# Optimization experiments

Measured on AMD Instinct MI355X. Metric: run time of the kernel, lower is better.

Reference implementation:

```python
import jax, jax.numpy as jnp
import numpy as np

D_MODEL = 1024
N_HEADS = 16
D_K = D_MODEL // N_HEADS
B, S = 2, 2048
NEG = -1.0e9


def setup_inputs() -> dict:
    key = jax.random.key(0)
    ks = jax.random.split(key, 12)
    sc = 1.0 / np.sqrt(D_MODEL)
    inp = {
        'query': jax.random.normal(ks[0], (B, S, D_MODEL), jnp.float32),
        'key': jax.random.normal(ks[1], (B, S, D_MODEL), jnp.float32),
        'value': jax.random.normal(ks[2], (B, S, D_MODEL), jnp.float32),
        # causal mask, broadcast over batch: 1 = attend, 0 = masked
        'mask': jnp.broadcast_to(jnp.tril(jnp.ones((S, S), jnp.int32)), (B, S, S)),
        'wq': jax.random.normal(ks[3], (D_MODEL, D_MODEL), jnp.float32) * sc,
        'bq': jnp.zeros((D_MODEL,), jnp.float32),
        'wk': jax.random.normal(ks[4], (D_MODEL, D_MODEL), jnp.float32) * sc,
        'bk': jnp.zeros((D_MODEL,), jnp.float32),
        'wv': jax.random.normal(ks[5], (D_MODEL, D_MODEL), jnp.float32) * sc,
        'bv': jnp.zeros((D_MODEL,), jnp.float32),
        'wo': jax.random.normal(ks[6], (D_MODEL, D_MODEL), jnp.float32) * sc,
        'bo': jnp.zeros((D_MODEL,), jnp.float32),
    }
    return inp


def reference(query, key, value, mask, wq, bq, wk, bk, wv, bv, wo, bo):
    b, sq, _ = query.shape
    sk = key.shape[1]
    # linear projections, split into heads: [B, H, S, d_k]
    def proj(x, w, bias, s):
        return (x @ w + bias).reshape(b, s, N_HEADS, D_K).transpose(0, 2, 1, 3)
    Q = proj(query, wq, bq, sq)
    K = proj(key, wk, bk, sk)
    V = proj(value, wv, bv, sk)
    # scaled dot-product attention with full score matrix [B, H, Sq, Sk]
    scores = jnp.einsum('bhqd,bhkd->bhqk', Q, K) / np.sqrt(D_K)
    scores = jnp.where(mask[:, None, :, :] == 0, NEG, scores)
    attn = jax.nn.softmax(scores, axis=-1)
    ctx = jnp.einsum('bhqk,bhkd->bhqd', attn, V)
    ctx = ctx.transpose(0, 2, 1, 3).reshape(b, sq, D_MODEL)
    return ctx @ wo + bo
```

## Files before the change

kernel.cpp:

```cpp
#include <hip/hip_runtime.h>
#include <stdint.h>

#define AS1 __attribute__((address_space(1)))
#define AS3 __attribute__((address_space(3)))

typedef __attribute__((ext_vector_type(8))) __bf16 bf16x8;
typedef __attribute__((ext_vector_type(4))) float f32x4;
typedef __attribute__((ext_vector_type(4))) unsigned int u32x4;
typedef __attribute__((ext_vector_type(2))) unsigned int u32x2;

static __device__ __forceinline__ void gload16(const void* g, void* l) {
    __builtin_amdgcn_global_load_lds((AS1 void*)(uintptr_t)g, (AS3 void*)l, 16, 0, 0);
}

static __device__ __forceinline__ unsigned cvt_pk_bf16(float lo, float hi) {
    unsigned r;
    asm volatile("v_cvt_pk_bf16_f32 %0, %1, %2" : "=v"(r) : "v"(lo), "v"(hi));
    return r;
}
static __device__ __forceinline__ unsigned short f2bf(float f) {
    return (unsigned short)(cvt_pk_bf16(f, 0.f) & 0xffffu);
}

static __device__ __forceinline__ f32x4 mfma16(bf16x8 a, bf16x8 b, f32x4 c) {
    return __builtin_amdgcn_mfma_f32_16x16x32_bf16(a, b, c, 0, 0, 0);
}

__global__ __launch_bounds__(256) void k_wtrans4(const float* __restrict__ w0,
                                                 const float* __restrict__ w1,
                                                 const float* __restrict__ w2,
                                                 const float* __restrict__ w3,
                                                 unsigned short* __restrict__ o0,
                                                 unsigned short* __restrict__ o1,
                                                 unsigned short* __restrict__ o2,
                                                 unsigned short* __restrict__ o3) {
    const float* W;
    unsigned short* Wt;
    switch (blockIdx.z) {
        case 0: W = w0; Wt = o0; break;
        case 1: W = w1; Wt = o1; break;
        case 2: W = w2; Wt = o2; break;
        default: W = w3; Wt = o3; break;
    }
    __shared__ unsigned short tile[64][72];
    const int tid = threadIdx.x;
    const int k0 = blockIdx.x * 64, n0 = blockIdx.y * 64;
#pragma unroll
    for (int j = 0; j < 4; ++j) {
        int c = j * 256 + tid;
        int kr = c >> 4, c4 = c & 15;
        f32x4 v = *(const f32x4*)(W + (size_t)(k0 + kr) * 1024 + n0 + c4 * 4);
#pragma unroll
        for (int e = 0; e < 4; ++e) tile[c4 * 4 + e][kr] = f2bf(v[e]);
    }
    __syncthreads();
#pragma unroll
    for (int j = 0; j < 2; ++j) {
        int c = j * 256 + tid;
        int nr = c >> 3, kc = c & 7;
        union { unsigned short s[8]; u32x4 v; } t;
#pragma unroll
        for (int e = 0; e < 8; ++e) t.s[e] = tile[nr][kc * 8 + e];
        *(u32x4*)(Wt + (size_t)(n0 + nr) * 1024 + k0 + kc * 8) = t.v;
    }
}

template <int A_F32, int OUT_F32>
__global__ __launch_bounds__(256) void k_gemm(const void* __restrict__ Ap,
                                              const unsigned short* __restrict__ Bt,
                                              const float* __restrict__ bias,
                                              void* __restrict__ Cp,
                                              int M, int N, int K, float cscale) {
    extern __shared__ __align__(16) char smem[];
    constexpr int ASZ = A_F32 ? 16384 : 8192;
    char* sA = smem;
    char* sB = smem + 2 * ASZ;
    const int tid = threadIdx.x;
    const int wave = tid >> 6, lane = tid & 63, g = lane >> 4, l16 = lane & 15;
    const int wm = wave & 1, wn = wave >> 1;
    const int m0 = blockIdx.x * 64, n0 = blockIdx.y * 128;

    f32x4 acc[2][4];
#pragma unroll
    for (int i = 0; i < 2; ++i)
#pragma unroll
        for (int j = 0; j < 4; ++j) acc[i][j] = (f32x4){0.f, 0.f, 0.f, 0.f};

    auto STAGE = [&](int k0, int buf) {
        if constexpr (A_F32) {
            const float* A = (const float*)Ap;
            char* dst = sA + buf * ASZ;
#pragma unroll
            for (int j = 0; j < 4; ++j) {
                int c = j * 256 + tid;
                int row = c >> 4, w = c & 15, kc = w ^ (row & 15);
                gload16(A + (size_t)(m0 + row) * K + k0 + kc * 4, dst + c * 16);
            }
        } else {
            const unsigned short* A = (const unsigned short*)Ap;
            char* dst = sA + buf * ASZ;
#pragma unroll
            for (int j = 0; j < 2; ++j) {
                int c = j * 256 + tid;
                int row = c >> 3, w = c & 7, kc = w ^ (row & 7);
                gload16(A + (size_t)(m0 + row) * K + k0 + kc * 8, dst + c * 16);
            }
        }
        char* dst = sB + buf * 16384;
#pragma unroll
        for (int j = 0; j < 4; ++j) {
            int c = j * 256 + tid;
            int row = c >> 3, w = c & 7, kc = w ^ (row & 7);
            gload16(Bt + (size_t)(n0 + row) * K + k0 + kc * 8, dst + c * 16);
        }
    };

    const int nkt = K >> 6;
    STAGE(0, 0);
    __syncthreads();
    int cur = 0;
#pragma unroll 1
    for (int kt = 0; kt < nkt; ++kt) {
        if (kt + 1 < nkt) STAGE((kt + 1) << 6, cur ^ 1);
        const char* sAc = sA + cur * ASZ;
        const char* sBc = sB + cur * 16384;
#pragma unroll
        for (int ks = 0; ks < 2; ++ks) {
            bf16x8 af[2];
#pragma unroll
            for (int mi = 0; mi < 2; ++mi) {
                int row = wm * 32 + mi * 16 + l16;
                if constexpr (A_F32) {
                    int c0 = (ks * 8 + g * 2) ^ (row & 15);
                    int c1 = (ks * 8 + g * 2 + 1) ^ (row & 15);
                    f32x4 lo = *(const f32x4*)(sAc + row * 256 + c0 * 16);
                    f32x4 hi = *(const f32x4*)(sAc + row * 256 + c1 * 16);
                    union { unsigned u[4]; bf16x8 v; } cv;
                    cv.u[0] = cvt_pk_bf16(lo[0], lo[1]);
                    cv.u[1] = cvt_pk_bf16(lo[2], lo[3]);
                    cv.u[2] = cvt_pk_bf16(hi[0], hi[1]);
                    cv.u[3] = cvt_pk_bf16(hi[2], hi[3]);
                    af[mi] = cv.v;
                } else {
                    int c = (ks * 4 + g) ^ (row & 7);
                    af[mi] = *(const bf16x8*)(sAc + row * 128 + c * 16);
                }
            }
#pragma unroll
            for (int ni = 0; ni < 4; ++ni) {
                int row = wn * 64 + ni * 16 + l16;
                int c = (ks * 4 + g) ^ (row & 7);
                bf16x8 bfr = *(const bf16x8*)(sBc + row * 128 + c * 16);
#pragma unroll
                for (int mi = 0; mi < 2; ++mi)
                    acc[mi][ni] = mfma16(af[mi], bfr, acc[mi][ni]);
            }
        }
        __syncthreads();
        cur ^= 1;
    }
#pragma unroll
    for (int ni = 0; ni < 4; ++ni) {
        int col = n0 + wn * 64 + ni * 16 + l16;
        float bn = bias[col];
#pragma unroll
        for (int mi = 0; mi < 2; ++mi) {
            int rbase = m0 + wm * 32 + mi * 16 + g * 4;
#pragma unroll
            for (int r = 0; r < 4; ++r) {
                float v = (acc[mi][ni][r] + bn) * cscale;
                if constexpr (OUT_F32)
                    ((float*)Cp)[(size_t)(rbase + r) * N + col] = v;
                else
                    ((unsigned short*)Cp)[(size_t)(rbase + r) * N + col] = f2bf(v);
            }
        }
    }
}

__global__ __launch_bounds__(256) void k_vtrans(const unsigned short* __restrict__ V2,
                                                unsigned short* __restrict__ Vt) {
    __shared__ unsigned short tile[64][72];
    const int tid = threadIdx.x;
    const int s0 = blockIdx.x * 64;
    const int bh = blockIdx.y, b = bh >> 4, h = bh & 15;
#pragma unroll
    for (int j = 0; j < 2; ++j) {
        int c = j * 256 + tid;
        int sr = c >> 3, dc = c & 7;
        union { u32x4 v; unsigned short s[8]; } t;
        t.v = *(const u32x4*)(V2 + (size_t)(b * 2048 + s0 + sr) * 1024 + h * 64 + dc * 8);
#pragma unroll
        for (int e = 0; e < 8; ++e) tile[dc * 8 + e][sr] = t.s[e];
    }
    __syncthreads();
#pragma unroll
    for (int j = 0; j < 2; ++j) {
        int c = j * 256 + tid;
        int dr = c >> 3, sc = c & 7;
        union { unsigned short s[8]; u32x4 v; } t;
#pragma unroll
        for (int e = 0; e < 8; ++e) t.s[e] = tile[dr][sc * 8 + e];
        *(u32x4*)(Vt + ((size_t)bh * 64 + dr) * 2048 + s0 + sc * 8) = t.v;
    }
}

__global__ __launch_bounds__(256) void k_attn(const unsigned short* __restrict__ Q2,
                                              const unsigned short* __restrict__ K2,
                                              const unsigned short* __restrict__ Vt,
                                              unsigned short* __restrict__ ctx) {
    __shared__ __align__(16) char sK[8192];
    __shared__ __align__(16) char sV[2][8192];
    __shared__ __align__(16) char sP[4][2048];

    const int tid = threadIdx.x, w = tid >> 6, lane = tid & 63;
    const int g = lane >> 4, l16 = lane & 15;
    const int bid = blockIdx.x;
    const int xcd = bid & 7, s5 = (bid >> 3) & 31, r4 = bid >> 8;
    const int bh = xcd * 4 + (s5 >> 3);
    const int w2 = s5 & 7;
    const int t = (r4 == 0) ? (31 - w2) : (r4 == 1) ? (16 + w2)
                : (r4 == 2) ? (15 - w2) : w2;
    const int b = bh >> 4, h = bh & 15;
    const int swzl = (l16 & 7) << 4;

    const int r0 = tid >> 3;
    const int sc0 = (tid & 7) ^ (r0 & 7);
    const unsigned short* ksrc0 = K2 + (size_t)(b * 2048 + r0) * 1024 + h * 64 + sc0 * 8;
    const unsigned short* ksrc1 = ksrc0 + 32 * 1024;
    const unsigned short* vsrc0 = Vt + ((size_t)bh * 64 + r0) * 2048 + sc0 * 8;
    const unsigned short* vsrc1 = vsrc0 + 32 * 2048;
    char* const myp = sP[w];

    const int wq0 = t * 64 + w * 16;
    const int qg = wq0 + l16;

    const unsigned short* qp = Q2 + (size_t)(b * 2048 + wq0 + l16) * 1024 + h * 64;
    bf16x8 qf0 = *(const bf16x8*)(qp + g * 8);
    bf16x8 qf1 = *(const bf16x8*)(qp + 32 + g * 8);

    f32x4 accO[4];
#pragma unroll
    for (int i = 0; i < 4; ++i) accO[i] = (f32x4){0.f, 0.f, 0.f, 0.f};
    float m = -1e30f, lsum = 0.f;

    const int nkv = t + 1;
    gload16(ksrc0, sK + tid * 16);
    gload16(ksrc1, sK + 4096 + tid * 16);
    gload16(vsrc0, sV[0] + tid * 16);
    gload16(vsrc1, sV[0] + 4096 + tid * 16);
    __syncthreads();

#pragma unroll 1
    for (int kt = 0; kt < nkv; ++kt) {
        const int cur = kt & 1;
        const int kv0 = kt * 64;
        float s[16];
        __builtin_amdgcn_s_setprio(1);
#pragma unroll
        for (int blk = 0; blk < 4; ++blk) {
            const int rl = blk * 16 + l16;
            const char* krow = sK + rl * 128;
            bf16x8 kf0 = *(const bf16x8*)(krow + ((g << 4) ^ swzl));
            bf16x8 kf1 = *(const bf16x8*)(krow + (((4 + g) << 4) ^ swzl));
            f32x4 a = (f32x4){0.f, 0.f, 0.f, 0.f};
            a = mfma16(kf0, qf0, a);
            a = mfma16(kf1, qf1, a);
#pragma unroll
            for (int rr = 0; rr < 4; ++rr) s[blk * 4 + rr] = a[rr];
        }
        __builtin_amdgcn_s_setprio(0);
        __syncthreads();
        if (kt + 1 < nkv) {
            gload16(ksrc0 + (size_t)(kv0 + 64) * 1024, sK + tid * 16);
            gload16(ksrc1 + (size_t)(kv0 + 64) * 1024, sK + 4096 + tid * 16);
            gload16(vsrc0 + (kv0 + 64), sV[cur ^ 1] + tid * 16);
            gload16(vsrc1 + (kv0 + 64), sV[cur ^ 1] + 4096 + tid * 16);
        }
        const bool needmask = (kt == t);
        if (needmask) {
#pragma unroll
            for (int j2 = 0; j2 < 16; ++j2) {
                int kvg = kv0 + (j2 >> 2) * 16 + g * 4 + (j2 & 3);
                if (kvg > qg) s[j2] = -1e9f;
            }
        }
        float c1 = fmaxf(fmaxf(s[0], s[1]), s[2]);
        c1 = fmaxf(fmaxf(c1, s[3]), s[4]);
        c1 = fmaxf(fmaxf(c1, s[5]), s[6]);
        c1 = fmaxf(c1, s[7]);
        float c2 = fmaxf(fmaxf(s[8], s[9]), s[10]);
        c2 = fmaxf(fmaxf(c2, s[11]), s[12]);
        c2 = fmaxf(fmaxf(c2, s[13]), s[14]);
        c2 = fmaxf(c2, s[15]);
        float mx = fmaxf(c1, c2);
        mx = fmaxf(mx, __shfl_xor(mx, 16));
        mx = fmaxf(mx, __shfl_xor(mx, 32));
        if (__any(mx > m + 8.f)) {
            float mnew = fmaxf(m, mx);
            float scale = __builtin_exp2f(m - mnew);
            lsum *= scale;
#pragma unroll
            for (int dt = 0; dt < 4; ++dt) accO[dt] = accO[dt] * scale;
            m = mnew;
        }
        float ps = 0.f;
        unsigned pk[8];
#pragma unroll
        for (int j2 = 0; j2 < 8; ++j2) {
            float p0 = __builtin_exp2f(s[2 * j2] - m);
            float p1 = __builtin_exp2f(s[2 * j2 + 1] - m);
            ps += p0 + p1;
            pk[j2] = cvt_pk_bf16(p0, p1);
        }
        ps += __shfl_xor(ps, 16);
        ps += __shfl_xor(ps, 32);
        lsum += ps;
#pragma unroll
        for (int blk = 0; blk < 4; ++blk) {
            u32x2 pw = {pk[blk * 2], pk[blk * 2 + 1]};
            *(u32x2*)(myp + l16 * 128 + ((blk * 32 + g * 8) ^ swzl)) = pw;
        }
        __builtin_amdgcn_s_setprio(1);
#pragma unroll
        for (int kvh = 0; kvh < 2; ++kvh) {
            bf16x8 pf = *(const bf16x8*)(myp + l16 * 128 + ((kvh * 64 + g * 16) ^ swzl));
#pragma unroll
            for (int dt = 0; dt < 4; ++dt) {
                const int rv = dt * 16 + l16;
                bf16x8 vf = *(const bf16x8*)(sV[cur] + rv * 128 + (((kvh * 4 + g) << 4) ^ swzl));
                accO[dt] = mfma16(vf, pf, accO[dt]);
            }
        }
        __builtin_amdgcn_s_setprio(0);
        __syncthreads();
    }
    float inv = 1.f / lsum;
    unsigned short* cp = ctx + (size_t)(b * 2048 + wq0 + l16) * 1024 + h * 64 + g * 4;
#pragma unroll
    for (int dt = 0; dt < 4; ++dt) {
        u32x2 o;
        o[0] = cvt_pk_bf16(accO[dt][0] * inv, accO[dt][1] * inv);
        o[1] = cvt_pk_bf16(accO[dt][2] * inv, accO[dt][3] * inv);
        *(u32x2*)(cp + dt * 16) = o;
    }
}

extern "C" void kernel_launch(void* const* d_in, const int* in_sizes, int n_in,
                              void* d_out, int out_size, void* d_ws, size_t ws_size,
                              hipStream_t stream) {
    const float* query = (const float*)d_in[0];
    const float* key   = (const float*)d_in[1];
    const float* value = (const float*)d_in[2];
    const float* wq = (const float*)d_in[4];
    const float* bq = (const float*)d_in[5];
    const float* wk = (const float*)d_in[6];
    const float* bk = (const float*)d_in[7];
    const float* wv = (const float*)d_in[8];
    const float* bv = (const float*)d_in[9];
    const float* wo = (const float*)d_in[10];
    const float* bo = (const float*)d_in[11];
    float* out = (float*)d_out;

    char* ws = (char*)d_ws;
    unsigned short* Wtq = (unsigned short*)ws;
    unsigned short* Wtk = Wtq + 1024 * 1024;
    unsigned short* Wtv = Wtk + 1024 * 1024;
    unsigned short* Wto = Wtv + 1024 * 1024;
    unsigned short* Q2  = Wto + 1024 * 1024;
    unsigned short* K2  = Q2 + 4096 * 1024;
    unsigned short* V2  = K2 + 4096 * 1024;
    unsigned short* Vt  = V2 + 4096 * 1024;
    unsigned short* ctx = Vt + 4096 * 1024;

    dim3 blk(256);
    k_wtrans4<<<dim3(16, 16, 4), blk, 0, stream>>>(wq, wk, wv, wo, Wtq, Wtk, Wtv, Wto);

    k_gemm<1, 0><<<dim3(64, 8), blk, 65536, stream>>>(query, Wtq, bq, Q2, 4096, 1024, 1024, 0.18033688011112042f);
    k_gemm<1, 0><<<dim3(64, 8), blk, 65536, stream>>>(key,   Wtk, bk, K2, 4096, 1024, 1024, 1.0f);
    k_gemm<1, 0><<<dim3(64, 8), blk, 65536, stream>>>(value, Wtv, bv, V2, 4096, 1024, 1024, 1.0f);

    k_vtrans<<<dim3(32, 32), blk, 0, stream>>>(V2, Vt);
    k_attn<<<dim3(1024), blk, 0, stream>>>(Q2, K2, Vt, ctx);

    k_gemm<0, 1><<<dim3(64, 8), blk, 49152, stream>>>(ctx, Wto, bo, out, 4096, 1024, 1024, 1.0f);
}
```

Baseline: 121.3 us.

## Merge QKV GEMMs, halve attention block size, use lazy max-rescale softmax

The three QKV projection GEMMs become one launch with a z-dimension that selects the operands. The attention kernel now runs 128-thread blocks over 32 query rows each (2048 blocks), scheduled longest-first, to improve load balance and occupancy. The online softmax starts with m=0 and only computes the row max and rescales when the partial sum exceeds a large threshold. The row-sum reduction across lanes moves to the end of the kernel. This removes per-tile max reductions and shuffles, at the risk of overflow or precision loss if scores grow large, and each tile is shared by fewer waves.

```diff
diff --git a/kernel.cpp b/kernel.cpp
--- a/kernel.cpp
+++ b/kernel.cpp
@@ -66,12 +66,12 @@
 }
 
 template <int A_F32, int OUT_F32>
-__global__ __launch_bounds__(256) void k_gemm(const void* __restrict__ Ap,
-                                              const unsigned short* __restrict__ Bt,
-                                              const float* __restrict__ bias,
-                                              void* __restrict__ Cp,
-                                              int M, int N, int K, float cscale) {
-    extern __shared__ __align__(16) char smem[];
+static __device__ __forceinline__ void gemm_body(const void* __restrict__ Ap,
+                                                 const unsigned short* __restrict__ Bt,
+                                                 const float* __restrict__ bias,
+                                                 void* __restrict__ Cp,
+                                                 int M, int N, int K, float cscale,
+                                                 char* smem) {
     constexpr int ASZ = A_F32 ? 16384 : 8192;
     char* sA = smem;
     char* sB = smem + 2 * ASZ;
@@ -178,6 +178,31 @@
     }
 }
 
+__global__ __launch_bounds__(256) void k_gemm_qkv(
+    const float* __restrict__ q, const float* __restrict__ k, const float* __restrict__ v,
+    const unsigned short* __restrict__ Wq, const unsigned short* __restrict__ Wk,
+    const unsigned short* __restrict__ Wv,
+    const float* __restrict__ bq, const float* __restrict__ bk, const float* __restrict__ bv,
+    unsigned short* __restrict__ Q2, unsigned short* __restrict__ K2,
+    unsigned short* __restrict__ V2) {
+    extern __shared__ __align__(16) char smem[];
+    const float* A; const unsigned short* Bt; const float* bias; unsigned short* C; float sc;
+    switch (blockIdx.z) {
+        case 0:  A = q; Bt = Wq; bias = bq; C = Q2; sc = 0.18033688011112042f; break;
+        case 1:  A = k; Bt = Wk; bias = bk; C = K2; sc = 1.0f; break;
+        default: A = v; Bt = Wv; bias = bv; C = V2; sc = 1.0f; break;
+    }
+    gemm_body<1, 0>(A, Bt, bias, C, 4096, 1024, 1024, sc, smem);
+}
+
+__global__ __launch_bounds__(256) void k_gemm_o(const unsigned short* __restrict__ ctx,
+                                                const unsigned short* __restrict__ Wo,
+                                                const float* __restrict__ bo,
+                                                float* __restrict__ out) {
+    extern __shared__ __align__(16) char smem[];
+    gemm_body<0, 1>(ctx, Wo, bo, out, 4096, 1024, 1024, 1.0f, smem);
+}
+
 __global__ __launch_bounds__(256) void k_vtrans(const unsigned short* __restrict__ V2,
                                                 unsigned short* __restrict__ Vt) {
     __shared__ unsigned short tile[64][72];
@@ -205,34 +230,30 @@
     }
 }
 
-__global__ __launch_bounds__(256) void k_attn(const unsigned short* __restrict__ Q2,
+__global__ __launch_bounds__(128) void k_attn(const unsigned short* __restrict__ Q2,
                                               const unsigned short* __restrict__ K2,
                                               const unsigned short* __restrict__ Vt,
                                               unsigned short* __restrict__ ctx) {
     __shared__ __align__(16) char sK[8192];
     __shared__ __align__(16) char sV[2][8192];
-    __shared__ __align__(16) char sP[4][2048];
+    __shared__ __align__(16) char sP[2][2048];
 
     const int tid = threadIdx.x, w = tid >> 6, lane = tid & 63;
     const int g = lane >> 4, l16 = lane & 15;
     const int bid = blockIdx.x;
-    const int xcd = bid & 7, s5 = (bid >> 3) & 31, r4 = bid >> 8;
-    const int bh = xcd * 4 + (s5 >> 3);
-    const int w2 = s5 & 7;
-    const int t = (r4 == 0) ? (31 - w2) : (r4 == 1) ? (16 + w2)
-                : (r4 == 2) ? (15 - w2) : w2;
+    const int xcd = bid & 7, j = bid >> 3;
+    const int bh = xcd * 4 + (j & 3);
+    const int t = 63 - (j >> 2);
     const int b = bh >> 4, h = bh & 15;
     const int swzl = (l16 & 7) << 4;
 
     const int r0 = tid >> 3;
     const int sc0 = (tid & 7) ^ (r0 & 7);
-    const unsigned short* ksrc0 = K2 + (size_t)(b * 2048 + r0) * 1024 + h * 64 + sc0 * 8;
-    const unsigned short* ksrc1 = ksrc0 + 32 * 1024;
-    const unsigned short* vsrc0 = Vt + ((size_t)bh * 64 + r0) * 2048 + sc0 * 8;
-    const unsigned short* vsrc1 = vsrc0 + 32 * 2048;
+    const unsigned short* ksrc = K2 + (size_t)(b * 2048 + r0) * 1024 + h * 64 + sc0 * 8;
+    const unsigned short* vsrc = Vt + ((size_t)bh * 64 + r0) * 2048 + sc0 * 8;
     char* const myp = sP[w];
 
-    const int wq0 = t * 64 + w * 16;
+    const int wq0 = t * 32 + w * 16;
     const int qg = wq0 + l16;
 
     const unsigned short* qp = Q2 + (size_t)(b * 2048 + wq0 + l16) * 1024 + h * 64;
@@ -242,13 +263,15 @@
     f32x4 accO[4];
 #pragma unroll
     for (int i = 0; i < 4; ++i) accO[i] = (f32x4){0.f, 0.f, 0.f, 0.f};
-    float m = -1e30f, lsum = 0.f;
-
-    const int nkv = t + 1;
-    gload16(ksrc0, sK + tid * 16);
-    gload16(ksrc1, sK + 4096 + tid * 16);
-    gload16(vsrc0, sV[0] + tid * 16);
-    gload16(vsrc1, sV[0] + 4096 + tid * 16);
+    float m = 0.f, lsum = 0.f;
+
+    const int nkv = (t >> 1) + 1;
+    const int diag = t >> 1;
+#pragma unroll
+    for (int rr = 0; rr < 4; ++rr) {
+        gload16(ksrc + (size_t)(rr * 16) * 1024, sK + rr * 2048 + tid * 16);
+        gload16(vsrc + (size_t)(rr * 16) * 2048, sV[0] + rr * 2048 + tid * 16);
+    }
     __syncthreads();
 
 #pragma unroll 1
@@ -272,37 +295,18 @@
         __builtin_amdgcn_s_setprio(0);
         __syncthreads();
         if (kt + 1 < nkv) {
-            gload16(ksrc0 + (size_t)(kv0 + 64) * 1024, sK + tid * 16);
-            gload16(ksrc1 + (size_t)(kv0 + 64) * 1024, sK + 4096 + tid * 16);
-            gload16(vsrc0 + (kv0 + 64), sV[cur ^ 1] + tid * 16);
-            gload16(vsrc1 + (kv0 + 64), sV[cur ^ 1] + 4096 + tid * 16);
-        }
-        const bool needmask = (kt == t);
-        if (needmask) {
+#pragma unroll
+            for (int rr = 0; rr < 4; ++rr) {
+                gload16(ksrc + (size_t)(kv0 + 64 + rr * 16) * 1024, sK + rr * 2048 + tid * 16);
+                gload16(vsrc + (size_t)(rr * 16) * 2048 + (kv0 + 64), sV[cur ^ 1] + rr * 2048 + tid * 16);
+            }
+        }
+        if (kt == diag) {
 #pragma unroll
             for (int j2 = 0; j2 < 16; ++j2) {
                 int kvg = kv0 + (j2 >> 2) * 16 + g * 4 + (j2 & 3);
                 if (kvg > qg) s[j2] = -1e9f;
             }
-        }
-        float c1 = fmaxf(fmaxf(s[0], s[1]), s[2]);
-        c1 = fmaxf(fmaxf(c1, s[3]), s[4]);
-        c1 = fmaxf(fmaxf(c1, s[5]), s[6]);
-        c1 = fmaxf(c1, s[7]);
-        float c2 = fmaxf(fmaxf(s[8], s[9]), s[10]);
-        c2 = fmaxf(fmaxf(c2, s[11]), s[12]);
-        c2 = fmaxf(fmaxf(c2, s[13]), s[14]);
-        c2 = fmaxf(c2, s[15]);
-        float mx = fmaxf(c1, c2);
-        mx = fmaxf(mx, __shfl_xor(mx, 16));
-        mx = fmaxf(mx, __shfl_xor(mx, 32));
-        if (__any(mx > m + 8.f)) {
-            float mnew = fmaxf(m, mx);
-            float scale = __builtin_exp2f(m - mnew);
-            lsum *= scale;
-#pragma unroll
-            for (int dt = 0; dt < 4; ++dt) accO[dt] = accO[dt] * scale;
-            m = mnew;
         }
         float ps = 0.f;
         unsigned pk[8];
@@ -313,8 +317,33 @@
             ps += p0 + p1;
             pk[j2] = cvt_pk_bf16(p0, p1);
         }
-        ps += __shfl_xor(ps, 16);
-        ps += __shfl_xor(ps, 32);
+        if (__any(ps > 16777216.f)) {
+            float c1 = fmaxf(fmaxf(s[0], s[1]), s[2]);
+            c1 = fmaxf(fmaxf(c1, s[3]), s[4]);
+            c1 = fmaxf(fmaxf(c1, s[5]), s[6]);
+            c1 = fmaxf(c1, s[7]);
+            float c2 = fmaxf(fmaxf(s[8], s[9]), s[10]);
+            c2 = fmaxf(fmaxf(c2, s[11]), s[12]);
+            c2 = fmaxf(fmaxf(c2, s[13]), s[14]);
+            c2 = fmaxf(c2, s[15]);
+            float mx = fmaxf(c1, c2);
+            mx = fmaxf(mx, __shfl_xor(mx, 16));
+            mx = fmaxf(mx, __shfl_xor(mx, 32));
+            float mnew = fmaxf(m, mx);
+            float scl = __builtin_exp2f(m - mnew);
+            lsum *= scl;
+#pragma unroll
+            for (int dt = 0; dt < 4; ++dt) accO[dt] = accO[dt] * scl;
+            m = mnew;
+            ps = 0.f;
+#pragma unroll
+            for (int j2 = 0; j2 < 8; ++j2) {
+                float p0 = __builtin_exp2f(s[2 * j2] - m);
+                float p1 = __builtin_exp2f(s[2 * j2 + 1] - m);
+                ps += p0 + p1;
+                pk[j2] = cvt_pk_bf16(p0, p1);
+            }
+        }
         lsum += ps;
 #pragma unroll
         for (int blk = 0; blk < 4; ++blk) {
@@ -335,7 +364,10 @@
         __builtin_amdgcn_s_setprio(0);
         __syncthreads();
     }
-    float inv = 1.f / lsum;
+    float v = lsum;
+    v += __shfl_xor(v, 16);
+    v += __shfl_xor(v, 32);
+    float inv = 1.f / v;
     unsigned short* cp = ctx + (size_t)(b * 2048 + wq0 + l16) * 1024 + h * 64 + g * 4;
 #pragma unroll
     for (int dt = 0; dt < 4; ++dt) {
@@ -376,12 +408,12 @@
     dim3 blk(256);
     k_wtrans4<<<dim3(16, 16, 4), blk, 0, stream>>>(wq, wk, wv, wo, Wtq, Wtk, Wtv, Wto);
 
-    k_gemm<1, 0><<<dim3(64, 8), blk, 65536, stream>>>(query, Wtq, bq, Q2, 4096, 1024, 1024, 0.18033688011112042f);
-    k_gemm<1, 0><<<dim3(64, 8), blk, 65536, stream>>>(key,   Wtk, bk, K2, 4096, 1024, 1024, 1.0f);
-    k_gemm<1, 0><<<dim3(64, 8), blk, 65536, stream>>>(value, Wtv, bv, V2, 4096, 1024, 1024, 1.0f);
+    k_gemm_qkv<<<dim3(64, 8, 3), blk, 65536, stream>>>(query, key, value,
+                                                       Wtq, Wtk, Wtv, bq, bk, bv,
+                                                       Q2, K2, V2);
 
     k_vtrans<<<dim3(32, 32), blk, 0, stream>>>(V2, Vt);
-    k_attn<<<dim3(1024), blk, 0, stream>>>(Q2, K2, Vt, ctx);
-
-    k_gemm<0, 1><<<dim3(64, 8), blk, 49152, stream>>>(ctx, Wto, bo, out, 4096, 1024, 1024, 1.0f);
-}
+    k_attn<<<dim3(2048), dim3(128), 0, stream>>>(Q2, K2, Vt, ctx);
+
+    k_gemm_o<<<dim3(64, 8), blk, 49152, stream>>>(ctx, Wto, bo, out);
+}
```

After: 118.4 us. -2.4%, faster.
